# Optimization experiments

Measured on AMD Instinct MI355X. Metric: run time of the kernel, lower is better.

## Reference

```python
import jax, jax.numpy as jnp
import numpy as np

B, N_P, N_S, D, H = 8, 512, 512, 512, 8
HD = D // H
SCALE = HD ** -0.5


def setup_inputs() -> dict:
    key = jax.random.key(0)
    ks = jax.random.split(key, 16)
    init = lambda k, shape, fan_in: jax.random.normal(k, shape, jnp.float32) * (1.0 / np.sqrt(fan_in))
    return {
        "piece_embeds": jax.random.normal(ks[0], (B, N_P, D), jnp.float32),
        "slot_embeds": jax.random.normal(ks[1], (B, N_S, D), jnp.float32),
        "mask": jax.random.randint(ks[2], (B, N_P, N_S), 0, 2, jnp.int32),
        "spatial_bias": jax.random.normal(ks[3], (B, N_P, N_S), jnp.float32),
        "Wq": init(ks[4], (D, D), D), "bq": jnp.zeros((D,), jnp.float32),
        "Wk": init(ks[5], (D, D), D), "bk": jnp.zeros((D,), jnp.float32),
        "Wv": init(ks[6], (D, D), D), "bv": jnp.zeros((D,), jnp.float32),
        "Wo": init(ks[7], (D, D), D), "bo": jnp.zeros((D,), jnp.float32),
        "Wc": init(ks[8], (2 * D,), 2 * D), "bc": jnp.zeros((), jnp.float32),
        "Wval": init(ks[9], (D,), D), "bval": jnp.zeros((), jnp.float32),
    }


def reference(piece_embeds, slot_embeds, mask, spatial_bias,
              Wq, bq, Wk, bk, Wv, bv, Wo, bo, Wc, bc, Wval, bval):
    Bv, Np, Dv = piece_embeds.shape
    Ns = slot_embeds.shape[1]
    Q = (piece_embeds @ Wq + bq).reshape(Bv, Np, H, HD)
    K = (slot_embeds @ Wk + bk).reshape(Bv, Ns, H, HD)
    V = (slot_embeds @ Wv + bv).reshape(Bv, Ns, H, HD)
    # per-head scores, scaled, then averaged over heads (non-standard)
    scores = jnp.einsum('bphd,bshd->bps', Q, K) * (SCALE / H)
    scores = scores + spatial_bias
    scores = jnp.where(mask == 0, jnp.float32(-1e9), scores)
    attn_probs = jax.nn.softmax(scores, axis=-1)  # dropout is identity at eval
    # the original expand*mul*sum over [B,Np,Ns,H,HD] == this contraction
    attn_output = jnp.einsum('bps,bshd->bphd', attn_probs, V).reshape(Bv, Np, Dv)
    output = attn_output @ Wo + bo
    value = (output.mean(axis=1) @ Wval + bval)[:, None]  # [B,1]
    # concat-linear over pairs == split-weight GEMMs with broadcast add
    Wc_p, Wc_s = Wc[:Dv], Wc[Dv:]
    compatibility = (piece_embeds @ Wc_p)[:, :, None] + (slot_embeds @ Wc_s)[:, None, :] + bc
    return scores, value, compatibility
```

## Files before the change

kernel.cpp:

```cpp
#include <hip/hip_runtime.h>
#include <math.h>

#define NP 512
#define NS 512
#define DD 512
#define INV64 0.015625f
#define NEGBIG -1000000000.0f
#define LOG2E 1.4426950408889634f

#define WS_SLOTBF 0
#define WS_WQBF   1048576
#define WS_WKBF   1179648
#define WS_MTBF   1310720
#define WS_WV     1441792
#define WS_U      1442304
#define WS_WQBK   1442816
#define WS_WKBQ   1443328
#define WS_VV     1443840
#define WS_A      1447936
#define WS_E      1452032
#define WS_CP     1456128
#define WS_CS     1460224
#define WS_Z      1464320
#define WS_W      1468416
#define WS_SC     1472512

#define OUT_SCORES 0
#define OUT_VALUE  2097152
#define OUT_COMP   2097160

typedef short bf16x8 __attribute__((ext_vector_type(8)));
typedef float f32x4 __attribute__((ext_vector_type(4)));

__device__ __forceinline__ short f2bf(float f) {
  unsigned u = __builtin_bit_cast(unsigned, f);
  u += 0x7fffu + ((u >> 16) & 1u);
  return (short)(u >> 16);
}

__device__ __forceinline__ void async_copy16(const void* g, void* l) {
  __builtin_amdgcn_global_load_lds(
      (const __attribute__((address_space(1))) unsigned int*)g,
      (__attribute__((address_space(3))) unsigned int*)l, 16, 0, 0);
}

__device__ __forceinline__ float dot8(float4 a0, float4 a1, float4 b0, float4 b1) {
  return a0.x * b0.x + a0.y * b0.y + a0.z * b0.z + a0.w * b0.w +
         a1.x * b1.x + a1.y * b1.y + a1.z * b1.z + a1.w * b1.w;
}

__device__ __forceinline__ float wave_red(float s) {
#pragma unroll
  for (int o = 32; o; o >>= 1) s += __shfl_xor(s, o);
  return s;
}

__device__ inline float wave_dot512(const float* __restrict__ x,
                                    const float* __restrict__ y, int lane) {
  float4 x0 = *(const float4*)&x[lane * 8];
  float4 x1 = *(const float4*)&x[lane * 8 + 4];
  float4 y0 = *(const float4*)&y[lane * 8];
  float4 y1 = *(const float4*)&y[lane * 8 + 4];
  return wave_red(dot8(x0, x1, y0, y1));
}

__global__ __launch_bounds__(256) void kA(
    const float* __restrict__ Wo, const float* __restrict__ Wval,
    const float* __restrict__ Wq, const float* __restrict__ bk,
    const float* __restrict__ Wk, const float* __restrict__ bq,
    const float* __restrict__ bo, const float* __restrict__ bval,
    float* __restrict__ ws, short* __restrict__ wqb, short* __restrict__ wkb) {
  int blk = blockIdx.x;
  if (blk < 385) {
    int wid = blk * 4 + (threadIdx.x >> 6);
    int lane = threadIdx.x & 63;
    if (wid >= 1538) return;
    const float *x, *y;
    float* dst;
    float extra = 0.f;
    int r = wid & 511;
    if (wid < 512)       { x = Wo + (size_t)r * DD; y = Wval; dst = ws + WS_WV + r; }
    else if (wid < 1024) { x = Wq + (size_t)r * DD; y = bk;   dst = ws + WS_WQBK + r; }
    else if (wid < 1536) { x = Wk + (size_t)r * DD; y = bq;   dst = ws + WS_WKBQ + r; }
    else if (wid == 1536){ x = bo; y = Wval; dst = ws + WS_SC + 1; extra = *bval; }
    else                 { x = bq; y = bk;   dst = ws + WS_SC + 2; }
    float s = wave_dot512(x, y, lane);
    if (lane == 0) *dst = s + extra;
  } else {
    int t = (blk - 385) * 256 + threadIdx.x;
    const float* src;
    short* dst;
    int off;
    if (t < 32768) { src = Wq; dst = wqb; off = t * 8; }
    else           { src = Wk; dst = wkb; off = (t - 32768) * 8; }
    float4 v0 = *(const float4*)&src[off];
    float4 v1 = *(const float4*)&src[off + 4];
    bf16x8 o;
    o[0] = f2bf(v0.x); o[1] = f2bf(v0.y); o[2] = f2bf(v0.z); o[3] = f2bf(v0.w);
    o[4] = f2bf(v1.x); o[5] = f2bf(v1.y); o[6] = f2bf(v1.z); o[7] = f2bf(v1.w);
    *(bf16x8*)&dst[off] = o;
  }
}

template <int NG>
__device__ __forceinline__ void stage_tile4(const short* __restrict__ G,
                                            short* lds, int r0, int k0, int wave,
                                            int lane) {
#pragma unroll
  for (int h = 0; h < NG / 256; ++h) {
    int s = h * 256 + wave * 64 + lane;
    int row = s >> 2;
    int g = (s & 3) ^ ((row >> 1) & 3);
    async_copy16(G + (size_t)(r0 + row) * DD + k0 + g * 8,
                 lds + (size_t)(h * 256 + wave * 64) * 8);
  }
}

__global__ __launch_bounds__(256) void kB(
    const float* __restrict__ Wv, const float* __restrict__ bv,
    const short* __restrict__ wkb, const short* __restrict__ wqb,
    float* __restrict__ ws, short* __restrict__ mtb) {
  __shared__ short As[2][128 * 32];
  __shared__ short Bs[2][64 * 32];
  if (blockIdx.x < 129) {
    int wid = blockIdx.x * 4 + (threadIdx.x >> 6);
    if (wid >= 513) return;
    int lane = threadIdx.x & 63;
    const float* wv = ws + WS_WV;
    const float *x, *y;
    float* dst;
    if (wid < 512) { x = Wv + (size_t)wid * DD; y = wv; dst = ws + WS_U + wid; }
    else           { x = bv; y = wv; dst = ws + WS_SC + 0; }
    float s = wave_dot512(x, y, lane);
    if (lane == 0) *dst = s;
    return;
  }
  int gb = blockIdx.x - 129;
  const int m0 = (gb & 3) * 128, n0 = (gb >> 2) * 64;
  const int wave = threadIdx.x >> 6, lane = threadIdx.x & 63;
  const int wr = wave >> 1, wc = wave & 1;
  const int li = lane & 15, g = lane >> 4;
  f32x4 acc[4][2] = {};
  stage_tile4<512>(wkb, &As[0][0], m0, 0, wave, lane);
  stage_tile4<256>(wqb, &Bs[0][0], n0, 0, wave, lane);
  __syncthreads();
  int buf = 0;
  for (int k0 = 0; k0 < DD; k0 += 32) {
    if (k0 + 32 < DD) {
      stage_tile4<512>(wkb, &As[buf ^ 1][0], m0, k0 + 32, wave, lane);
      stage_tile4<256>(wqb, &Bs[buf ^ 1][0], n0, k0 + 32, wave, lane);
    }
    bf16x8 af[4], bfr[2];
#pragma unroll
    for (int am = 0; am < 4; ++am) {
      int row = wr * 64 + am * 16 + li;
      int gp = g ^ ((row >> 1) & 3);
      af[am] = *(const bf16x8*)&As[buf][row * 32 + gp * 8];
    }
#pragma unroll
    for (int bn = 0; bn < 2; ++bn) {
      int row = wc * 32 + bn * 16 + li;
      int gp = g ^ ((row >> 1) & 3);
      bfr[bn] = *(const bf16x8*)&Bs[buf][row * 32 + gp * 8];
    }
#pragma unroll
    for (int am = 0; am < 4; ++am)
#pragma unroll
      for (int bn = 0; bn < 2; ++bn)
        acc[am][bn] = __builtin_amdgcn_mfma_f32_16x16x32_bf16(
            af[am], bfr[bn], acc[am][bn], 0, 0, 0);
    __syncthreads();
    buf ^= 1;
  }
#pragma unroll
  for (int am = 0; am < 4; ++am)
#pragma unroll
    for (int i = 0; i < 4; ++i) {
      int grow = m0 + wr * 64 + am * 16 + g * 4 + i;
#pragma unroll
      for (int bn = 0; bn < 2; ++bn) {
        int gcol = n0 + wc * 32 + bn * 16 + li;
        mtb[(size_t)grow * DD + gcol] = f2bf(acc[am][bn][i]);
      }
    }
}

__global__ __launch_bounds__(256) void kC(
    const float* __restrict__ piece, const float* __restrict__ slot,
    const float* __restrict__ Wc, float* __restrict__ ws,
    short* __restrict__ pbf, short* __restrict__ sbf) {
  int lane = threadIdx.x & 63;
  if (blockIdx.x < 1024) {
    int wid = blockIdx.x * 4 + (threadIdx.x >> 6);
    const float* row = piece + (size_t)wid * DD;
    float4 x0 = *(const float4*)&row[lane * 8];
    float4 x1 = *(const float4*)&row[lane * 8 + 4];
    bf16x8 o;
    o[0] = f2bf(x0.x); o[1] = f2bf(x0.y); o[2] = f2bf(x0.z); o[3] = f2bf(x0.w);
    o[4] = f2bf(x1.x); o[5] = f2bf(x1.y); o[6] = f2bf(x1.z); o[7] = f2bf(x1.w);
    *(bf16x8*)&pbf[(size_t)wid * DD + lane * 8] = o;
    const float* y = ws + WS_WQBK;
    float4 y0 = *(const float4*)&y[lane * 8];
    float4 y1 = *(const float4*)&y[lane * 8 + 4];
    float4 c0 = *(const float4*)&Wc[lane * 8];
    float4 c1 = *(const float4*)&Wc[lane * 8 + 4];
    float da = wave_red(dot8(x0, x1, y0, y1));
    float dc = wave_red(dot8(x0, x1, c0, c1));
    if (lane == 0) { ws[WS_A + wid] = da; ws[WS_CP + wid] = dc; }
  } else if (blockIdx.x < 2048) {
    int wid = (blockIdx.x - 1024) * 4 + (threadIdx.x >> 6);
    const float* row = slot + (size_t)wid * DD;
    float4 x0 = *(const float4*)&row[lane * 8];
    float4 x1 = *(const float4*)&row[lane * 8 + 4];
    bf16x8 o;
    o[0] = f2bf(x0.x); o[1] = f2bf(x0.y); o[2] = f2bf(x0.z); o[3] = f2bf(x0.w);
    o[4] = f2bf(x1.x); o[5] = f2bf(x1.y); o[6] = f2bf(x1.z); o[7] = f2bf(x1.w);
    *(bf16x8*)&sbf[(size_t)wid * DD + lane * 8] = o;
    const float* y = ws + WS_WKBQ;
    float4 y0 = *(const float4*)&y[lane * 8];
    float4 y1 = *(const float4*)&y[lane * 8 + 4];
    const float* u = ws + WS_U;
    float4 u0 = *(const float4*)&u[lane * 8];
    float4 u1 = *(const float4*)&u[lane * 8 + 4];
    const float* c = Wc + DD;
    float4 c0 = *(const float4*)&c[lane * 8];
    float4 c1 = *(const float4*)&c[lane * 8 + 4];
    float de = wave_red(dot8(x0, x1, y0, y1));
    float dv = wave_red(dot8(x0, x1, u0, u1));
    float dc = wave_red(dot8(x0, x1, c0, c1));
    if (lane == 0) {
      ws[WS_E + wid] = de;
      ws[WS_VV + wid] = dv + ws[WS_SC + 0];
      ws[WS_CS + wid] = dc;
    }
  } else {
    float4 zz = make_float4(0.f, 0.f, 0.f, 0.f);
#pragma unroll
    for (int k = 0; k < 8; ++k)
      *(float4*)&ws[WS_Z + (threadIdx.x * 8 + k) * 4] = zz;
  }
}

template <int MODE>
__global__ __launch_bounds__(512) void k_gemm8(
    const short* __restrict__ A, const short* __restrict__ B,
    short* __restrict__ Cb, const float* __restrict__ ws_,
    const float* __restrict__ sbias, const int* __restrict__ maskp,
    float* __restrict__ out, float* __restrict__ zarr,
    float* __restrict__ warr) {
  __shared__ short As[2][128 * 64];
  __shared__ short Bs[2][64 * 64];
  const int wave = threadIdx.x >> 6, lane = threadIdx.x & 63;
  const int wr = wave >> 1, wc = wave & 1;
  const int li = lane & 15, g = lane >> 4;
  const int id = blockIdx.x;
  int b, m0, n0;
  if (MODE == 0) { b = 0; m0 = (id & 31) * 128; n0 = (id >> 5) * 64; }
  else           { b = id & 7; m0 = ((id >> 3) & 3) * 128; n0 = (id >> 5) * 64; }
  const short* Ab = A + (size_t)b * NP * DD;
  const short* Bb = B + (size_t)b * NS * DD;
  f32x4 acc[2][2] = {};

  auto stage = [&](int bufi, int k0) {
#pragma unroll
    for (int h = 0; h < 2; ++h) {
      int s = h * 512 + wave * 64 + lane;
      int row = s >> 3;
      int gsrc = (s & 7) ^ (row & 7);
      async_copy16(Ab + (size_t)(m0 + row) * DD + k0 + gsrc * 8,
                   &As[bufi][(h * 512 + wave * 64) * 8]);
    }
    {
      int s = wave * 64 + lane;
      int row = s >> 3;
      int gsrc = (s & 7) ^ (row & 7);
      async_copy16(Bb + (size_t)(n0 + row) * DD + k0 + gsrc * 8,
                   &Bs[bufi][(wave * 64) * 8]);
    }
  };

  stage(0, 0);
  __syncthreads();
  int buf = 0;
  for (int k0 = 0; k0 < DD; k0 += 64) {
    if (k0 + 64 < DD) stage(buf ^ 1, k0 + 64);
    bf16x8 af[2][2], bfv[2][2];
#pragma unroll
    for (int kk = 0; kk < 2; ++kk) {
#pragma unroll
      for (int am = 0; am < 2; ++am) {
        int row = wr * 32 + am * 16 + li;
        int slot = row * 8 + ((kk * 4 + g) ^ (row & 7));
        af[am][kk] = *(const bf16x8*)&As[buf][slot * 8];
      }
#pragma unroll
      for (int bn = 0; bn < 2; ++bn) {
        int row = wc * 32 + bn * 16 + li;
        int slot = row * 8 + ((kk * 4 + g) ^ (row & 7));
        bfv[bn][kk] = *(const bf16x8*)&Bs[buf][slot * 8];
      }
    }
#pragma unroll
    for (int kk = 0; kk < 2; ++kk)
#pragma unroll
      for (int am = 0; am < 2; ++am)
#pragma unroll
        for (int bn = 0; bn < 2; ++bn)
          acc[am][bn] = __builtin_amdgcn_mfma_f32_16x16x32_bf16(
              af[am][kk], bfv[bn][kk], acc[am][bn], 0, 0, 0);
    __syncthreads();
    buf ^= 1;
  }

  if (MODE == 0) {
#pragma unroll
    for (int am = 0; am < 2; ++am)
#pragma unroll
      for (int i = 0; i < 4; ++i) {
        int grow = m0 + wr * 32 + am * 16 + g * 4 + i;
#pragma unroll
        for (int bn = 0; bn < 2; ++bn) {
          int gcol = n0 + wc * 32 + bn * 16 + li;
          Cb[(size_t)grow * DD + gcol] = f2bf(acc[am][bn][i]);
        }
      }
  } else {
    const float sbb = ws_[WS_SC + 2];
    const float* evp = ws_ + WS_E + b * NS;
    const float* vvp = ws_ + WS_VV + b * NS;
    const float* avp = ws_ + WS_A + b * NP;
    float ev[2], vvl[2];
#pragma unroll
    for (int bn = 0; bn < 2; ++bn) {
      int scol = n0 + wc * 32 + bn * 16 + li;
      ev[bn] = evp[scol];
      vvl[bn] = vvp[scol];
    }
#pragma unroll
    for (int am = 0; am < 2; ++am)
#pragma unroll
      for (int i = 0; i < 4; ++i) {
        int p = m0 + wr * 32 + am * 16 + g * 4 + i;
        float av = avp[p] + sbb;
        float zp = 0.f, wp = 0.f;
#pragma unroll
        for (int bn = 0; bn < 2; ++bn) {
          int scol = n0 + wc * 32 + bn * 16 + li;
          size_t idx = ((size_t)b * NP + p) * NS + scol;
          float v = fmaf(acc[am][bn][i] + av + ev[bn], INV64, sbias[idx]);
          v = (maskp[idx] == 0) ? NEGBIG : v;
          out[OUT_SCORES + idx] = v;
          float e = exp2f(v * LOG2E);
          zp += e;
          wp += e * vvl[bn];
        }
#pragma unroll
        for (int o = 1; o < 16; o <<= 1) {
          zp += __shfl_xor(zp, o);
          wp += __shfl_xor(wp, o);
        }
        if (li == 0) {
          atomicAdd(&zarr[b * NP + p], zp);
          atomicAdd(&warr[b * NP + p], wp);
        }
      }
  }
}

__global__ __launch_bounds__(256) void kG(const float* __restrict__ ws,
                                          const float* __restrict__ bc,
                                          float* __restrict__ out) {
  if (blockIdx.x < 2048) {
    int idx = blockIdx.x * 256 + threadIdx.x;
    int lin = idx << 2;
    int s = lin & (NS - 1);
    int p = (lin >> 9) & (NP - 1);
    int bb = lin >> 18;
    float cp = ws[WS_CP + bb * NP + p];
    float4 cs = *(const float4*)&ws[WS_CS + bb * NS + s];
    float bcv = *bc;
    float4 o = make_float4(cp + cs.x + bcv, cp + cs.y + bcv, cp + cs.z + bcv,
                           cp + cs.w + bcv);
    *(float4*)&out[OUT_COMP + lin] = o;
  } else {
    int tid = threadIdx.x;
    int bb = tid >> 5, j = tid & 31;
    const float* zp = ws + WS_Z + bb * NP;
    const float* wp = ws + WS_W + bb * NP;
    float s = 0.f;
#pragma unroll
    for (int k = 0; k < 16; ++k) {
      int p = k * 32 + j;
      s += wp[p] / zp[p];
    }
#pragma unroll
    for (int o = 16; o; o >>= 1) s += __shfl_xor(s, o);
    if (j == 0) out[OUT_VALUE + bb] = s * (1.0f / NP) + ws[WS_SC + 1];
  }
}

extern "C" void kernel_launch(void* const* d_in, const int* in_sizes, int n_in,
                              void* d_out, int out_size, void* d_ws,
                              size_t ws_size, hipStream_t stream) {
  const float* piece = (const float*)d_in[0];
  const float* slot = (const float*)d_in[1];
  const int* mask = (const int*)d_in[2];
  const float* sbias = (const float*)d_in[3];
  const float* Wq = (const float*)d_in[4];
  const float* bq = (const float*)d_in[5];
  const float* Wk = (const float*)d_in[6];
  const float* bk = (const float*)d_in[7];
  const float* Wv = (const float*)d_in[8];
  const float* bv = (const float*)d_in[9];
  const float* Wo = (const float*)d_in[10];
  const float* bo = (const float*)d_in[11];
  const float* Wc = (const float*)d_in[12];
  const float* bc = (const float*)d_in[13];
  const float* Wval = (const float*)d_in[14];
  const float* bval = (const float*)d_in[15];
  float* out = (float*)d_out;
  float* ws = (float*)d_ws;

  short* pbf = (short*)out;
  short* tbf = (short*)(out + OUT_COMP);
  short* sbf = (short*)(ws + WS_SLOTBF);
  short* wqb = (short*)(ws + WS_WQBF);
  short* wkb = (short*)(ws + WS_WKBF);
  short* mtb = (short*)(ws + WS_MTBF);

  hipLaunchKernelGGL(kA, dim3(641), dim3(256), 0, stream,
                     Wo, Wval, Wq, bk, Wk, bq, bo, bval, ws, wqb, wkb);
  hipLaunchKernelGGL(kB, dim3(161), dim3(256), 0, stream, Wv, bv, wkb, wqb, ws, mtb);
  hipLaunchKernelGGL(kC, dim3(2049), dim3(256), 0, stream, piece, slot, Wc, ws, pbf, sbf);
  hipLaunchKernelGGL((k_gemm8<0>), dim3(256), dim3(512), 0, stream,
                     pbf, mtb, tbf, (const float*)nullptr, (const float*)nullptr,
                     (const int*)nullptr, (float*)nullptr, (float*)nullptr,
                     (float*)nullptr);
  hipLaunchKernelGGL((k_gemm8<1>), dim3(256), dim3(512), 0, stream,
                     tbf, sbf, (short*)nullptr, ws, sbias, mask, out,
                     ws + WS_Z, ws + WS_W);
  hipLaunchKernelGGL(kG, dim3(2049), dim3(256), 0, stream, ws, bc, out);
}
```

Before: 52.86 us.

## Unify GEMMs into 64x64 tiled kernel and fuse compatibility write into scores epilogue

Replaces the separate 128x64 weight GEMM and 128x64 batched GEMMs with one templated 64x64-tile kernel used in three modes, which doubles the block count for the large GEMMs. The compatibility broadcast output is now written in the scores GEMM epilogue, and the final kernel shrinks to the value reduction only. This removes one full pass over the 8 MB compatibility output. Intermediate bf16 buffers move from the output buffer into workspace, which needs a larger workspace, and the smaller tiles mean more operand reloads per output.

```diff
diff --git a/kernel.cpp b/kernel.cpp
--- a/kernel.cpp
+++ b/kernel.cpp
@@ -8,22 +8,24 @@
 #define NEGBIG -1000000000.0f
 #define LOG2E 1.4426950408889634f
 
-#define WS_SLOTBF 0
-#define WS_WQBF   1048576
-#define WS_WKBF   1179648
-#define WS_MTBF   1310720
-#define WS_WV     1441792
-#define WS_U      1442304
-#define WS_WQBK   1442816
-#define WS_WKBQ   1443328
-#define WS_VV     1443840
-#define WS_A      1447936
-#define WS_E      1452032
-#define WS_CP     1456128
-#define WS_CS     1460224
-#define WS_Z      1464320
-#define WS_W      1468416
-#define WS_SC     1472512
+#define WS_MTBF   0
+#define WS_TBF    131072
+#define WS_PBF    1179648
+#define WS_SBF    2228224
+#define WS_WQBF   3276800
+#define WS_WKBF   3407872
+#define WS_WV     3538944
+#define WS_U      3539456
+#define WS_WQBK   3539968
+#define WS_WKBQ   3540480
+#define WS_VV     3540992
+#define WS_A      3545088
+#define WS_E      3549184
+#define WS_CP     3553280
+#define WS_CS     3557376
+#define WS_Z      3561472
+#define WS_W      3565568
+#define WS_SC     3569664
 
 #define OUT_SCORES 0
 #define OUT_VALUE  2097152
@@ -79,11 +81,11 @@
     float* dst;
     float extra = 0.f;
     int r = wid & 511;
-    if (wid < 512)       { x = Wo + (size_t)r * DD; y = Wval; dst = ws + WS_WV + r; }
-    else if (wid < 1024) { x = Wq + (size_t)r * DD; y = bk;   dst = ws + WS_WQBK + r; }
-    else if (wid < 1536) { x = Wk + (size_t)r * DD; y = bq;   dst = ws + WS_WKBQ + r; }
-    else if (wid == 1536){ x = bo; y = Wval; dst = ws + WS_SC + 1; extra = *bval; }
-    else                 { x = bq; y = bk;   dst = ws + WS_SC + 2; }
+    if (wid < 512)        { x = Wo + (size_t)r * DD; y = Wval; dst = ws + WS_WV + r; }
+    else if (wid < 1024)  { x = Wq + (size_t)r * DD; y = bk;   dst = ws + WS_WQBK + r; }
+    else if (wid < 1536)  { x = Wk + (size_t)r * DD; y = bq;   dst = ws + WS_WKBQ + r; }
+    else if (wid == 1536) { x = bo; y = Wval; dst = ws + WS_SC + 1; extra = *bval; }
+    else                  { x = bq; y = bk;   dst = ws + WS_SC + 2; }
     float s = wave_dot512(x, y, lane);
     if (lane == 0) *dst = s + extra;
   } else {
@@ -102,87 +104,137 @@
   }
 }
 
-template <int NG>
-__device__ __forceinline__ void stage_tile4(const short* __restrict__ G,
-                                            short* lds, int r0, int k0, int wave,
-                                            int lane) {
-#pragma unroll
-  for (int h = 0; h < NG / 256; ++h) {
-    int s = h * 256 + wave * 64 + lane;
-    int row = s >> 2;
-    int g = (s & 3) ^ ((row >> 1) & 3);
-    async_copy16(G + (size_t)(r0 + row) * DD + k0 + g * 8,
-                 lds + (size_t)(h * 256 + wave * 64) * 8);
-  }
-}
-
-__global__ __launch_bounds__(256) void kB(
-    const float* __restrict__ Wv, const float* __restrict__ bv,
-    const short* __restrict__ wkb, const short* __restrict__ wqb,
-    float* __restrict__ ws, short* __restrict__ mtb) {
-  __shared__ short As[2][128 * 32];
-  __shared__ short Bs[2][64 * 32];
-  if (blockIdx.x < 129) {
-    int wid = blockIdx.x * 4 + (threadIdx.x >> 6);
-    if (wid >= 513) return;
-    int lane = threadIdx.x & 63;
-    const float* wv = ws + WS_WV;
-    const float *x, *y;
-    float* dst;
-    if (wid < 512) { x = Wv + (size_t)wid * DD; y = wv; dst = ws + WS_U + wid; }
-    else           { x = bv; y = wv; dst = ws + WS_SC + 0; }
-    float s = wave_dot512(x, y, lane);
-    if (lane == 0) *dst = s;
+template <int MODE>
+__global__ __launch_bounds__(256) void k64(
+    const short* __restrict__ A, const short* __restrict__ B,
+    short* __restrict__ Cb, const float* __restrict__ Wv,
+    const float* __restrict__ bv, float* __restrict__ ws,
+    const float* __restrict__ sbias, const int* __restrict__ maskp,
+    const float* __restrict__ bc, float* __restrict__ out) {
+  __shared__ alignas(16) short As[2][64 * 64];
+  __shared__ alignas(16) short Bs[2][64 * 64];
+  const int wave = threadIdx.x >> 6, lane = threadIdx.x & 63;
+  const int id = blockIdx.x;
+
+  if (MODE == 0 && id >= 64) {
+    int wid = (id - 64) * 4 + wave;
+    if (wid > 512) return;
+    if (wid < 512) {
+      float s = wave_dot512(Wv + (size_t)wid * DD, ws + WS_WV, lane);
+      if (lane == 0) ws[WS_U + wid] = s;
+    } else {
+      float s = wave_dot512(bv, ws + WS_WV, lane);
+      if (lane == 0) ws[WS_SC + 0] = s;
+    }
     return;
   }
-  int gb = blockIdx.x - 129;
-  const int m0 = (gb & 3) * 128, n0 = (gb >> 2) * 64;
-  const int wave = threadIdx.x >> 6, lane = threadIdx.x & 63;
+
   const int wr = wave >> 1, wc = wave & 1;
   const int li = lane & 15, g = lane >> 4;
-  f32x4 acc[4][2] = {};
-  stage_tile4<512>(wkb, &As[0][0], m0, 0, wave, lane);
-  stage_tile4<256>(wqb, &Bs[0][0], n0, 0, wave, lane);
+  int b = 0, m0, n0;
+  if (MODE == 0)      { m0 = (id & 7) * 64; n0 = (id >> 3) * 64; }
+  else if (MODE == 1) { m0 = (id & 63) * 64; n0 = (id >> 6) * 64; }
+  else                { b = id & 7; m0 = ((id >> 6) & 7) * 64; n0 = ((id >> 3) & 7) * 64; }
+  const short* Ab = A + (size_t)b * NP * DD;
+  const short* Bb = B + (size_t)b * NS * DD;
+  f32x4 acc[2][2] = {};
+
+  auto stage = [&](int bufi, int k0) {
+#pragma unroll
+    for (int h = 0; h < 2; ++h) {
+      int s = h * 256 + threadIdx.x;
+      int row = s >> 3;
+      int gsrc = (s & 7) ^ (row & 7);
+      async_copy16(Ab + (size_t)(m0 + row) * DD + k0 + gsrc * 8, &As[bufi][s * 8]);
+      async_copy16(Bb + (size_t)(n0 + row) * DD + k0 + gsrc * 8, &Bs[bufi][s * 8]);
+    }
+  };
+
+  stage(0, 0);
   __syncthreads();
   int buf = 0;
-  for (int k0 = 0; k0 < DD; k0 += 32) {
-    if (k0 + 32 < DD) {
-      stage_tile4<512>(wkb, &As[buf ^ 1][0], m0, k0 + 32, wave, lane);
-      stage_tile4<256>(wqb, &Bs[buf ^ 1][0], n0, k0 + 32, wave, lane);
-    }
-    bf16x8 af[4], bfr[2];
-#pragma unroll
-    for (int am = 0; am < 4; ++am) {
-      int row = wr * 64 + am * 16 + li;
-      int gp = g ^ ((row >> 1) & 3);
-      af[am] = *(const bf16x8*)&As[buf][row * 32 + gp * 8];
-    }
-#pragma unroll
-    for (int bn = 0; bn < 2; ++bn) {
-      int row = wc * 32 + bn * 16 + li;
-      int gp = g ^ ((row >> 1) & 3);
-      bfr[bn] = *(const bf16x8*)&Bs[buf][row * 32 + gp * 8];
-    }
-#pragma unroll
-    for (int am = 0; am < 4; ++am)
-#pragma unroll
-      for (int bn = 0; bn < 2; ++bn)
-        acc[am][bn] = __builtin_amdgcn_mfma_f32_16x16x32_bf16(
-            af[am], bfr[bn], acc[am][bn], 0, 0, 0);
+  for (int k0 = 0; k0 < DD; k0 += 64) {
+    if (k0 + 64 < DD) stage(buf ^ 1, k0 + 64);
+    bf16x8 af[2][2], bfv[2][2];
+#pragma unroll
+    for (int kk = 0; kk < 2; ++kk) {
+#pragma unroll
+      for (int am = 0; am < 2; ++am) {
+        int row = wr * 32 + am * 16 + li;
+        af[am][kk] = *(const bf16x8*)&As[buf][(row * 8 + ((kk * 4 + g) ^ (row & 7))) * 8];
+      }
+#pragma unroll
+      for (int bn = 0; bn < 2; ++bn) {
+        int row = wc * 32 + bn * 16 + li;
+        bfv[bn][kk] = *(const bf16x8*)&Bs[buf][(row * 8 + ((kk * 4 + g) ^ (row & 7))) * 8];
+      }
+    }
+#pragma unroll
+    for (int kk = 0; kk < 2; ++kk)
+#pragma unroll
+      for (int am = 0; am < 2; ++am)
+#pragma unroll
+        for (int bn = 0; bn < 2; ++bn)
+          acc[am][bn] = __builtin_amdgcn_mfma_f32_16x16x32_bf16(
+              af[am][kk], bfv[bn][kk], acc[am][bn], 0, 0, 0);
     __syncthreads();
     buf ^= 1;
   }
-#pragma unroll
-  for (int am = 0; am < 4; ++am)
-#pragma unroll
-    for (int i = 0; i < 4; ++i) {
-      int grow = m0 + wr * 64 + am * 16 + g * 4 + i;
-#pragma unroll
-      for (int bn = 0; bn < 2; ++bn) {
-        int gcol = n0 + wc * 32 + bn * 16 + li;
-        mtb[(size_t)grow * DD + gcol] = f2bf(acc[am][bn][i]);
+
+  if (MODE != 2) {
+#pragma unroll
+    for (int am = 0; am < 2; ++am)
+#pragma unroll
+      for (int i = 0; i < 4; ++i) {
+        int grow = m0 + wr * 32 + am * 16 + g * 4 + i;
+#pragma unroll
+        for (int bn = 0; bn < 2; ++bn) {
+          int gcol = n0 + wc * 32 + bn * 16 + li;
+          Cb[(size_t)grow * DD + gcol] = f2bf(acc[am][bn][i]);
+        }
       }
-    }
+  } else {
+    const float sbb = ws[WS_SC + 2];
+    const float bcv = *bc;
+    float ev[2], vvl[2], csl[2];
+#pragma unroll
+    for (int bn = 0; bn < 2; ++bn) {
+      int scol = n0 + wc * 32 + bn * 16 + li;
+      ev[bn] = ws[WS_E + b * NS + scol];
+      vvl[bn] = ws[WS_VV + b * NS + scol];
+      csl[bn] = ws[WS_CS + b * NS + scol];
+    }
+#pragma unroll
+    for (int am = 0; am < 2; ++am)
+#pragma unroll
+      for (int i = 0; i < 4; ++i) {
+        int p = m0 + wr * 32 + am * 16 + g * 4 + i;
+        float av = ws[WS_A + b * NP + p] + sbb;
+        float cpv = ws[WS_CP + b * NP + p] + bcv;
+        float zp = 0.f, wp = 0.f;
+#pragma unroll
+        for (int bn = 0; bn < 2; ++bn) {
+          int scol = n0 + wc * 32 + bn * 16 + li;
+          size_t idx = ((size_t)b * NP + p) * NS + scol;
+          float v = fmaf(acc[am][bn][i] + av + ev[bn], INV64, sbias[idx]);
+          v = (maskp[idx] == 0) ? NEGBIG : v;
+          out[OUT_SCORES + idx] = v;
+          float ee = exp2f(v * LOG2E);
+          zp += ee;
+          wp += ee * vvl[bn];
+          out[OUT_COMP + idx] = cpv + csl[bn];
+        }
+#pragma unroll
+        for (int o = 1; o < 16; o <<= 1) {
+          zp += __shfl_xor(zp, o);
+          wp += __shfl_xor(wp, o);
+        }
+        if (li == 0) {
+          atomicAdd(&ws[WS_Z + b * NP + p], zp);
+          atomicAdd(&ws[WS_W + b * NP + p], wp);
+        }
+      }
+  }
 }
 
 __global__ __launch_bounds__(256) void kC(
@@ -241,162 +293,20 @@
   }
 }
 
-template <int MODE>
-__global__ __launch_bounds__(512) void k_gemm8(
-    const short* __restrict__ A, const short* __restrict__ B,
-    short* __restrict__ Cb, const float* __restrict__ ws_,
-    const float* __restrict__ sbias, const int* __restrict__ maskp,
-    float* __restrict__ out, float* __restrict__ zarr,
-    float* __restrict__ warr) {
-  __shared__ short As[2][128 * 64];
-  __shared__ short Bs[2][64 * 64];
-  const int wave = threadIdx.x >> 6, lane = threadIdx.x & 63;
-  const int wr = wave >> 1, wc = wave & 1;
-  const int li = lane & 15, g = lane >> 4;
-  const int id = blockIdx.x;
-  int b, m0, n0;
-  if (MODE == 0) { b = 0; m0 = (id & 31) * 128; n0 = (id >> 5) * 64; }
-  else           { b = id & 7; m0 = ((id >> 3) & 3) * 128; n0 = (id >> 5) * 64; }
-  const short* Ab = A + (size_t)b * NP * DD;
-  const short* Bb = B + (size_t)b * NS * DD;
-  f32x4 acc[2][2] = {};
-
-  auto stage = [&](int bufi, int k0) {
-#pragma unroll
-    for (int h = 0; h < 2; ++h) {
-      int s = h * 512 + wave * 64 + lane;
-      int row = s >> 3;
-      int gsrc = (s & 7) ^ (row & 7);
-      async_copy16(Ab + (size_t)(m0 + row) * DD + k0 + gsrc * 8,
-                   &As[bufi][(h * 512 + wave * 64) * 8]);
-    }
-    {
-      int s = wave * 64 + lane;
-      int row = s >> 3;
-      int gsrc = (s & 7) ^ (row & 7);
-      async_copy16(Bb + (size_t)(n0 + row) * DD + k0 + gsrc * 8,
-                   &Bs[bufi][(wave * 64) * 8]);
-    }
-  };
-
-  stage(0, 0);
-  __syncthreads();
-  int buf = 0;
-  for (int k0 = 0; k0 < DD; k0 += 64) {
-    if (k0 + 64 < DD) stage(buf ^ 1, k0 + 64);
-    bf16x8 af[2][2], bfv[2][2];
-#pragma unroll
-    for (int kk = 0; kk < 2; ++kk) {
-#pragma unroll
-      for (int am = 0; am < 2; ++am) {
-        int row = wr * 32 + am * 16 + li;
-        int slot = row * 8 + ((kk * 4 + g) ^ (row & 7));
-        af[am][kk] = *(const bf16x8*)&As[buf][slot * 8];
-      }
-#pragma unroll
-      for (int bn = 0; bn < 2; ++bn) {
-        int row = wc * 32 + bn * 16 + li;
-        int slot = row * 8 + ((kk * 4 + g) ^ (row & 7));
-        bfv[bn][kk] = *(const bf16x8*)&Bs[buf][slot * 8];
-      }
-    }
-#pragma unroll
-    for (int kk = 0; kk < 2; ++kk)
-#pragma unroll
-      for (int am = 0; am < 2; ++am)
-#pragma unroll
-        for (int bn = 0; bn < 2; ++bn)
-          acc[am][bn] = __builtin_amdgcn_mfma_f32_16x16x32_bf16(
-              af[am][kk], bfv[bn][kk], acc[am][bn], 0, 0, 0);
-    __syncthreads();
-    buf ^= 1;
-  }
-
-  if (MODE == 0) {
-#pragma unroll
-    for (int am = 0; am < 2; ++am)
-#pragma unroll
-      for (int i = 0; i < 4; ++i) {
-        int grow = m0 + wr * 32 + am * 16 + g * 4 + i;
-#pragma unroll
-        for (int bn = 0; bn < 2; ++bn) {
-          int gcol = n0 + wc * 32 + bn * 16 + li;
-          Cb[(size_t)grow * DD + gcol] = f2bf(acc[am][bn][i]);
-        }
-      }
-  } else {
-    const float sbb = ws_[WS_SC + 2];
-    const float* evp = ws_ + WS_E + b * NS;
-    const float* vvp = ws_ + WS_VV + b * NS;
-    const float* avp = ws_ + WS_A + b * NP;
-    float ev[2], vvl[2];
-#pragma unroll
-    for (int bn = 0; bn < 2; ++bn) {
-      int scol = n0 + wc * 32 + bn * 16 + li;
-      ev[bn] = evp[scol];
-      vvl[bn] = vvp[scol];
-    }
-#pragma unroll
-    for (int am = 0; am < 2; ++am)
-#pragma unroll
-      for (int i = 0; i < 4; ++i) {
-        int p = m0 + wr * 32 + am * 16 + g * 4 + i;
-        float av = avp[p] + sbb;
-        float zp = 0.f, wp = 0.f;
-#pragma unroll
-        for (int bn = 0; bn < 2; ++bn) {
-          int scol = n0 + wc * 32 + bn * 16 + li;
-          size_t idx = ((size_t)b * NP + p) * NS + scol;
-          float v = fmaf(acc[am][bn][i] + av + ev[bn], INV64, sbias[idx]);
-          v = (maskp[idx] == 0) ? NEGBIG : v;
-          out[OUT_SCORES + idx] = v;
-          float e = exp2f(v * LOG2E);
-          zp += e;
-          wp += e * vvl[bn];
-        }
-#pragma unroll
-        for (int o = 1; o < 16; o <<= 1) {
-          zp += __shfl_xor(zp, o);
-          wp += __shfl_xor(wp, o);
-        }
-        if (li == 0) {
-          atomicAdd(&zarr[b * NP + p], zp);
-          atomicAdd(&warr[b * NP + p], wp);
-        }
-      }
-  }
-}
-
-__global__ __launch_bounds__(256) void kG(const float* __restrict__ ws,
-                                          const float* __restrict__ bc,
+__global__ __launch_bounds__(512) void kG(const float* __restrict__ ws,
                                           float* __restrict__ out) {
-  if (blockIdx.x < 2048) {
-    int idx = blockIdx.x * 256 + threadIdx.x;
-    int lin = idx << 2;
-    int s = lin & (NS - 1);
-    int p = (lin >> 9) & (NP - 1);
-    int bb = lin >> 18;
-    float cp = ws[WS_CP + bb * NP + p];
-    float4 cs = *(const float4*)&ws[WS_CS + bb * NS + s];
-    float bcv = *bc;
-    float4 o = make_float4(cp + cs.x + bcv, cp + cs.y + bcv, cp + cs.z + bcv,
-                           cp + cs.w + bcv);
-    *(float4*)&out[OUT_COMP + lin] = o;
-  } else {
-    int tid = threadIdx.x;
-    int bb = tid >> 5, j = tid & 31;
-    const float* zp = ws + WS_Z + bb * NP;
-    const float* wp = ws + WS_W + bb * NP;
-    float s = 0.f;
-#pragma unroll
-    for (int k = 0; k < 16; ++k) {
-      int p = k * 32 + j;
-      s += wp[p] / zp[p];
-    }
-#pragma unroll
-    for (int o = 16; o; o >>= 1) s += __shfl_xor(s, o);
-    if (j == 0) out[OUT_VALUE + bb] = s * (1.0f / NP) + ws[WS_SC + 1];
-  }
+  int vb = threadIdx.x >> 6, l = threadIdx.x & 63;
+  const float* zp = ws + WS_Z + vb * NP;
+  const float* wp = ws + WS_W + vb * NP;
+  float s = 0.f;
+#pragma unroll
+  for (int j = 0; j < 8; ++j) {
+    int p = l + j * 64;
+    s += wp[p] / zp[p];
+  }
+#pragma unroll
+  for (int o = 32; o; o >>= 1) s += __shfl_xor(s, o);
+  if (l == 0) out[OUT_VALUE + vb] = s * (1.0f / NP) + ws[WS_SC + 1];
 }
 
 extern "C" void kernel_launch(void* const* d_in, const int* in_sizes, int n_in,
@@ -421,23 +331,27 @@
   float* out = (float*)d_out;
   float* ws = (float*)d_ws;
 
-  short* pbf = (short*)out;
-  short* tbf = (short*)(out + OUT_COMP);
-  short* sbf = (short*)(ws + WS_SLOTBF);
+  short* mtb = (short*)(ws + WS_MTBF);
+  short* tbf = (short*)(ws + WS_TBF);
+  short* pbf = (short*)(ws + WS_PBF);
+  short* sbf = (short*)(ws + WS_SBF);
   short* wqb = (short*)(ws + WS_WQBF);
   short* wkb = (short*)(ws + WS_WKBF);
-  short* mtb = (short*)(ws + WS_MTBF);
 
   hipLaunchKernelGGL(kA, dim3(641), dim3(256), 0, stream,
                      Wo, Wval, Wq, bk, Wk, bq, bo, bval, ws, wqb, wkb);
-  hipLaunchKernelGGL(kB, dim3(161), dim3(256), 0, stream, Wv, bv, wkb, wqb, ws, mtb);
-  hipLaunchKernelGGL(kC, dim3(2049), dim3(256), 0, stream, piece, slot, Wc, ws, pbf, sbf);
-  hipLaunchKernelGGL((k_gemm8<0>), dim3(256), dim3(512), 0, stream,
+  hipLaunchKernelGGL((k64<0>), dim3(193), dim3(256), 0, stream,
+                     wkb, wqb, mtb, Wv, bv, ws,
+                     (const float*)nullptr, (const int*)nullptr,
+                     (const float*)nullptr, (float*)nullptr);
+  hipLaunchKernelGGL(kC, dim3(2049), dim3(256), 0, stream, piece, slot, Wc, ws,
+                     pbf, sbf);
+  hipLaunchKernelGGL((k64<1>), dim3(512), dim3(256), 0, stream,
                      pbf, mtb, tbf, (const float*)nullptr, (const float*)nullptr,
-                     (const int*)nullptr, (float*)nullptr, (float*)nullptr,
-                     (float*)nullptr);
-  hipLaunchKernelGGL((k_gemm8<1>), dim3(256), dim3(512), 0, stream,
-                     tbf, sbf, (short*)nullptr, ws, sbias, mask, out,
-                     ws + WS_Z, ws + WS_W);
-  hipLaunchKernelGGL(kG, dim3(2049), dim3(256), 0, stream, ws, bc, out);
-}
+                     ws, (const float*)nullptr, (const int*)nullptr,
+                     (const float*)nullptr, (float*)nullptr);
+  hipLaunchKernelGGL((k64<2>), dim3(512), dim3(256), 0, stream,
+                     tbf, sbf, (short*)nullptr, (const float*)nullptr,
+                     (const float*)nullptr, ws, sbias, mask, bc, out);
+  hipLaunchKernelGGL(kG, dim3(1), dim3(512), 0, stream, ws, out);
+}
```

After: 48.86 us. 1.08x faster.
